# Optimization experiments

Hardware: AMD Instinct MI355X
Metric: run time of the kernel (lower is better)

## Reference

```python
import jax, jax.numpy as jnp
import numpy as np

N_NODES = 50000
N_EDGES = 600000
DIM = 128
VOCAB = 512
PAD_ID = 0
LN_EPS = 1e-5


def setup_inputs() -> dict:
    key = jax.random.key(0)
    ks = jax.random.split(key, 8)
    node_ids = jax.random.randint(ks[0], (N_NODES,), 0, VOCAB, dtype=jnp.int32)
    edge_index = jax.random.randint(ks[1], (2, N_EDGES), 0, N_NODES, dtype=jnp.int32)
    edge_weight = jax.random.uniform(ks[2], (N_EDGES,), dtype=jnp.float32)
    # embedding with padding row zeroed (padding_idx semantics)
    emb = jax.random.normal(ks[3], (VOCAB, DIM), dtype=jnp.float32) * 0.05
    emb = emb.at[PAD_ID].set(0.0)
    s = 1.0 / np.sqrt(DIM)
    W1 = jax.random.normal(ks[4], (DIM, DIM), dtype=jnp.float32) * s
    b1 = jnp.zeros((DIM,), jnp.float32)
    W2 = jax.random.normal(ks[5], (DIM, DIM), dtype=jnp.float32) * s
    b2 = jnp.zeros((DIM,), jnp.float32)
    return {
        "node_ids": node_ids, "edge_index": edge_index, "edge_weight": edge_weight,
        "emb": emb, "W1": W1, "b1": b1, "W2": W2, "b2": b2,
        "gamma1": jnp.ones((DIM,), jnp.float32), "beta1": jnp.zeros((DIM,), jnp.float32),
        "gamma2": jnp.ones((DIM,), jnp.float32), "beta2": jnp.zeros((DIM,), jnp.float32),
    }


def _gcn_conv(x, row, col, ew, W, b, n_nodes):
    """PyG GCNConv: normalize=True, add_self_loops=True, improved=False.
    Aggregation j->i: edge (row=src j, col=dst i)."""
    h = x @ W  # [N, out]
    # add self loops with weight 1
    loop = jnp.arange(n_nodes, dtype=row.dtype)
    row_f = jnp.concatenate([row, loop])
    col_f = jnp.concatenate([col, loop])
    ew_f = jnp.concatenate([ew, jnp.ones((n_nodes,), ew.dtype)])
    # symmetric degree normalization (deg over destination index)
    deg = jax.ops.segment_sum(ew_f, col_f, num_segments=n_nodes)
    dis = jnp.where(deg > 0, jax.lax.rsqrt(jnp.maximum(deg, 1e-12)), 0.0)
    norm = dis[row_f] * ew_f * dis[col_f]  # [E+N]
    msg = norm[:, None] * h[row_f]  # gather + scale  [E+N, out]
    out = jax.ops.segment_sum(msg, col_f, num_segments=n_nodes)  # scatter-add
    return out + b


def _layer_norm(x, gamma, beta):
    mu = jnp.mean(x, axis=-1, keepdims=True)
    var = jnp.mean(jnp.square(x - mu), axis=-1, keepdims=True)
    return (x - mu) * jax.lax.rsqrt(var + LN_EPS) * gamma + beta


def reference(node_ids, edge_index, edge_weight, emb, W1, b1, W2, b2,
              gamma1, beta1, gamma2, beta2):
    row, col = edge_index[0], edge_index[1]
    x = emb[node_ids]  # [N, D]
    x1 = _gcn_conv(x, row, col, edge_weight, W1, b1, N_NODES)
    x = _layer_norm(x + x1, gamma1, beta1)  # dropout is identity in eval
    x2 = _gcn_conv(x, row, col, edge_weight, W2, b2, N_NODES)
    x = _layer_norm(x + x2, gamma2, beta2)
    return x
```

## Files before the change

### kernel.cpp

```cpp
#include <hip/hip_runtime.h>

#define N_NODES 50000
#define N_EDGES 600000
#define DIM     128
#define VOCAB   512
#define LN_EPS  1e-5f
#define FIXS    16777216.0f

typedef unsigned int uint;
typedef unsigned long long ull;

__device__ __forceinline__ uint f2bf(float f) {
    uint u = __float_as_uint(f);
    return (u + 0x7fffu + ((u >> 16) & 1u)) >> 16;
}
__device__ __forceinline__ float bf_lo(uint p) { return __uint_as_float(p << 16); }
__device__ __forceinline__ float bf_hi(uint p) { return __uint_as_float(p & 0xffff0000u); }

__global__ void deg_rank_kernel(const int* __restrict__ ei, const float* __restrict__ ew,
                                ull* pack, int* __restrict__ rank, int E) {
    int e0 = (blockIdx.x * blockDim.x + threadIdx.x) * 4;
    if (e0 >= E) return;
    int4   c = *(const int4*)  (ei + E + e0);
    float4 w = *(const float4*)(ew + e0);
    ull a0 = (1ull << 32) | (ull)(uint)__float2int_rn(w.x * FIXS);
    ull a1 = (1ull << 32) | (ull)(uint)__float2int_rn(w.y * FIXS);
    ull a2 = (1ull << 32) | (ull)(uint)__float2int_rn(w.z * FIXS);
    ull a3 = (1ull << 32) | (ull)(uint)__float2int_rn(w.w * FIXS);
    ull r0 = atomicAdd(&pack[c.x], a0);
    ull r1 = atomicAdd(&pack[c.y], a1);
    ull r2 = atomicAdd(&pack[c.z], a2);
    ull r3 = atomicAdd(&pack[c.w], a3);
    *(int4*)(rank + e0) = make_int4((int)(r0 >> 32), (int)(r1 >> 32),
                                    (int)(r2 >> 32), (int)(r3 >> 32));
}

__global__ void scan_a(const ull* __restrict__ pack,
                       float* dis, int* row_ptr, int* bsum, int n) {
    __shared__ int sd[1024];
    int t = threadIdx.x;
    int i = blockIdx.x * 1024 + t;
    int v = 0;
    if (i < n) {
        ull pv = pack[i];
        v = (int)(pv >> 32);
        dis[i] = rsqrtf(1.0f + (float)(uint)(pv & 0xffffffffu) * (1.0f / FIXS));
    }
    sd[t] = v;
    __syncthreads();
    for (int off = 1; off < 1024; off <<= 1) {
        int add = (t >= off) ? sd[t - off] : 0;
        __syncthreads();
        sd[t] += add;
        __syncthreads();
    }
    if (i < n) row_ptr[i] = sd[t] - v;
    if (t == 1023) bsum[blockIdx.x] = sd[t];
}

__global__ void scan_b(const int* __restrict__ bsum, int* bofs, int nb) {
    int t = threadIdx.x;
    int v = (t < nb) ? bsum[t] : 0;
    int incl = v;
    #pragma unroll
    for (int off = 1; off < 64; off <<= 1) {
        int up = __shfl_up(incl, off, 64);
        if (t >= off) incl += up;
    }
    if (t < nb) bofs[t] = incl - v;
}

__global__ void scan_c(int* row_ptr, const int* __restrict__ bofs, int n, int E) {
    int i = blockIdx.x * 1024 + threadIdx.x;
    if (i < n) row_ptr[i] += bofs[blockIdx.x];
    if (i == 0) row_ptr[n] = E;
}

__global__ void scatter_kernel(const int* __restrict__ ei, const float* __restrict__ ew,
                               const float* __restrict__ dis, const int* __restrict__ nid,
                               const int* __restrict__ row_ptr, const int* __restrict__ rank,
                               int2* __restrict__ epack, int E) {
    int e = blockIdx.x * blockDim.x + threadIdx.x;
    if (e < E) {
        int s = ei[e];
        int c = ei[E + e];
        int pos = row_ptr[c] + rank[e];
        uint ids = (uint)s | ((uint)nid[s] << 16);
        float wp = dis[s] * ew[e];
        epack[pos] = make_int2((int)ids, __float_as_int(wp));
    }
}

template<bool XBF>
__global__ __launch_bounds__(256) void matmul128(const void* __restrict__ Xv,
                                                 const float* __restrict__ W,
                                                 uint* __restrict__ Hb, int M) {
    __shared__ float Wt[32 * 128];
    __shared__ float Xt[64 * 36];
    int tid = threadIdx.x;
    int tx = tid & 31, ty = tid >> 5;
    int r0 = blockIdx.x * 64;
    float acc[8][4];
    #pragma unroll
    for (int j = 0; j < 8; j++)
        #pragma unroll
        for (int c = 0; c < 4; c++) acc[j][c] = 0.f;

    for (int kb = 0; kb < 128; kb += 32) {
        __syncthreads();
        #pragma unroll
        for (int q = 0; q < 4; q++) {
            int f = q * 256 + tid;
            ((float4*)Wt)[f] = *(const float4*)(W + kb * 128 + f * 4);
        }
        #pragma unroll
        for (int q = 0; q < 2; q++) {
            int f = q * 256 + tid;
            int row = f >> 3, cs = f & 7;
            int gr = r0 + row;
            float4 xv = make_float4(0.f, 0.f, 0.f, 0.f);
            if (gr < M) {
                if (XBF) {
                    uint2 xp = *(const uint2*)((const uint*)Xv + (size_t)gr * 64 + kb / 2 + cs * 2);
                    xv = make_float4(bf_lo(xp.x), bf_hi(xp.x), bf_lo(xp.y), bf_hi(xp.y));
                } else {
                    xv = *(const float4*)((const float*)Xv + (size_t)gr * 128 + kb + cs * 4);
                }
            }
            *(float4*)(Xt + row * 36 + cs * 4) = xv;
        }
        __syncthreads();
        #pragma unroll
        for (int k = 0; k < 32; k += 4) {
            float wv[4][4];
            #pragma unroll
            for (int kk = 0; kk < 4; kk++) {
                float4 t4 = *(const float4*)(Wt + (k + kk) * 128 + tx * 4);
                wv[kk][0] = t4.x; wv[kk][1] = t4.y; wv[kk][2] = t4.z; wv[kk][3] = t4.w;
            }
            #pragma unroll
            for (int j = 0; j < 8; j++) {
                float4 xv = *(const float4*)(Xt + (ty * 8 + j) * 36 + k);
                float xs[4] = {xv.x, xv.y, xv.z, xv.w};
                #pragma unroll
                for (int kk = 0; kk < 4; kk++)
                    #pragma unroll
                    for (int c = 0; c < 4; c++)
                        acc[j][c] = fmaf(xs[kk], wv[kk][c], acc[j][c]);
            }
        }
    }
    #pragma unroll
    for (int j = 0; j < 8; j++) {
        int gr = r0 + ty * 8 + j;
        if (gr < M) {
            uint p0 = f2bf(acc[j][0]) | (f2bf(acc[j][1]) << 16);
            uint p1 = f2bf(acc[j][2]) | (f2bf(acc[j][3]) << 16);
            ((uint2*)Hb)[(size_t)gr * 32 + tx] = make_uint2(p0, p1);
        }
    }
}

template<int SHIFT, bool RESID_BF, bool OUT_BF>
__global__ __launch_bounds__(256) void agg_ln(const int* __restrict__ row_ptr,
                                              const int2* __restrict__ epack,
                                              const float* __restrict__ dis,
                                              const uint* __restrict__ hb,
                                              const int* __restrict__ nid,
                                              const void* __restrict__ resid,
                                              const float* __restrict__ bias,
                                              const float* __restrict__ gamma,
                                              const float* __restrict__ beta,
                                              void* __restrict__ out, int n) {
    int i = (blockIdx.x * 256 + threadIdx.x) >> 6;
    int lane = threadIdx.x & 63;
    if (i >= n) return;
    int hri = nid ? nid[i] : i;
    float dl = dis[i];
    uint ps = hb[(size_t)hri * 64 + lane];
    float acc0 = dl * bf_lo(ps);
    float acc1 = dl * bf_hi(ps);
    float c0 = 0.f, c1 = 0.f;
    int e0 = row_ptr[i], e1 = row_ptr[i + 1];
    int j = e0;
    for (; j + 3 < e1; j += 4) {
        int2 r0 = epack[j], r1 = epack[j + 1], r2 = epack[j + 2], r3 = epack[j + 3];
        uint q0 = hb[(size_t)(((uint)r0.x >> SHIFT) & 0xffffu) * 64 + lane];
        uint q1 = hb[(size_t)(((uint)r1.x >> SHIFT) & 0xffffu) * 64 + lane];
        uint q2 = hb[(size_t)(((uint)r2.x >> SHIFT) & 0xffffu) * 64 + lane];
        uint q3 = hb[(size_t)(((uint)r3.x >> SHIFT) & 0xffffu) * 64 + lane];
        float w0 = __int_as_float(r0.y), w1 = __int_as_float(r1.y);
        float w2 = __int_as_float(r2.y), w3 = __int_as_float(r3.y);
        acc0 += w0 * bf_lo(q0); acc1 += w0 * bf_hi(q0);
        c0   += w1 * bf_lo(q1); c1   += w1 * bf_hi(q1);
        acc0 += w2 * bf_lo(q2); acc1 += w2 * bf_hi(q2);
        c0   += w3 * bf_lo(q3); c1   += w3 * bf_hi(q3);
    }
    for (; j < e1; ++j) {
        int2 r = epack[j];
        float w = __int_as_float(r.y);
        uint q = hb[(size_t)(((uint)r.x >> SHIFT) & 0xffffu) * 64 + lane];
        acc0 += w * bf_lo(q); acc1 += w * bf_hi(q);
    }
    acc0 += c0; acc1 += c1;
    float2 xr;
    if (RESID_BF) {
        uint pr = ((const uint*)resid)[(size_t)hri * 64 + lane];
        xr = make_float2(bf_lo(pr), bf_hi(pr));
    } else {
        xr = ((const float2*)resid)[(size_t)hri * 64 + lane];
    }
    float2 bi = ((const float2*)bias)[lane];
    float v0 = xr.x + dl * acc0 + bi.x;
    float v1 = xr.y + dl * acc1 + bi.y;
    float s1 = v0 + v1, s2 = v0 * v0 + v1 * v1;
    #pragma unroll
    for (int o = 32; o > 0; o >>= 1) {
        s1 += __shfl_xor(s1, o, 64);
        s2 += __shfl_xor(s2, o, 64);
    }
    float mu   = s1 * (1.0f / DIM);
    float var  = s2 * (1.0f / DIM) - mu * mu;
    float rstd = rsqrtf(var + LN_EPS);
    float2 ga = ((const float2*)gamma)[lane];
    float2 be = ((const float2*)beta)[lane];
    float o0 = (v0 - mu) * rstd * ga.x + be.x;
    float o1 = (v1 - mu) * rstd * ga.y + be.y;
    if (OUT_BF) {
        ((uint*)out)[(size_t)i * 64 + lane] = f2bf(o0) | (f2bf(o1) << 16);
    } else {
        ((float2*)out)[(size_t)i * 64 + lane] = make_float2(o0, o1);
    }
}

extern "C" void kernel_launch(void* const* d_in, const int* in_sizes, int n_in,
                              void* d_out, int out_size, void* d_ws, size_t ws_size,
                              hipStream_t stream) {
    const int*   node_ids = (const int*)  d_in[0];
    const int*   ei       = (const int*)  d_in[1];
    const float* ew       = (const float*)d_in[2];
    const float* emb      = (const float*)d_in[3];
    const float* W1       = (const float*)d_in[4];
    const float* b1       = (const float*)d_in[5];
    const float* W2       = (const float*)d_in[6];
    const float* b2       = (const float*)d_in[7];
    const float* g1       = (const float*)d_in[8];
    const float* be1      = (const float*)d_in[9];
    const float* g2       = (const float*)d_in[10];
    const float* be2      = (const float*)d_in[11];
    float* out = (float*)d_out;

    char* p = (char*)d_ws;
    auto alloc = [&](size_t bytes) {
        char* r = p;
        p += (bytes + 255) & ~(size_t)255;
        return r;
    };
    uint*  h2b     = (uint*) alloc((size_t)N_NODES * 64 * 4);
    uint*  x1b     = (uint*) alloc((size_t)N_NODES * 64 * 4);
    uint*  hembB   = (uint*) alloc((size_t)VOCAB * 64 * 4);
    ull*   pack    = (ull*)  alloc((size_t)N_NODES * 8);
    float* disv    = (float*)alloc((size_t)N_NODES * 4);
    int*   row_ptr = (int*)  alloc((size_t)(N_NODES + 1) * 4);
    int*   rank    = (int*)  alloc((size_t)N_EDGES * 4);
    int*   bsum    = (int*)  alloc(64 * 4);
    int*   bofs    = (int*)  alloc(64 * 4);
    int2*  epack   = (int2*) alloc((size_t)N_EDGES * 8);

    int nb = (N_NODES + 1023) / 1024;

    hipMemsetAsync(pack, 0, (size_t)N_NODES * 8, stream);
    deg_rank_kernel<<<(N_EDGES / 4 + 255) / 256, 256, 0, stream>>>(ei, ew, pack, rank, N_EDGES);
    scan_a<<<nb, 1024, 0, stream>>>(pack, disv, row_ptr, bsum, N_NODES);
    scan_b<<<1, 64, 0, stream>>>(bsum, bofs, nb);
    scan_c<<<nb, 1024, 0, stream>>>(row_ptr, bofs, N_NODES, N_EDGES);
    scatter_kernel<<<(N_EDGES + 255) / 256, 256, 0, stream>>>(ei, ew, disv, node_ids,
                                                              row_ptr, rank, epack, N_EDGES);

    matmul128<false><<<(VOCAB + 63) / 64, 256, 0, stream>>>(emb, W1, hembB, VOCAB);
    agg_ln<16, false, true><<<(N_NODES + 3) / 4, 256, 0, stream>>>(
        row_ptr, epack, disv, hembB, node_ids, emb, b1, g1, be1, x1b, N_NODES);

    matmul128<true><<<(N_NODES + 63) / 64, 256, 0, stream>>>(x1b, W2, h2b, N_NODES);
    agg_ln<0, true, false><<<(N_NODES + 3) / 4, 256, 0, stream>>>(
        row_ptr, epack, disv, h2b, nullptr, x1b, b2, g2, be2, out, N_NODES);
}
```

Baseline: 252.2 us.

## Use bf16 MFMA for second-layer matmul and widen aggregation gather batching

Replaces the FP32 shared-memory SIMT matmul for the 50000x128x128 second-layer projection with a bf16 MFMA kernel. W2 is prepacked into an MFMA-friendly bf16 layout by a small extra kernel, and the already-bf16 activations are fed directly. The aggregation loop now issues 8 edge-record and gather loads per iteration, with masked tails and 4 independent accumulators, to expose more memory-level parallelism. W2 is quantised to bf16, which adds rounding error. The MFMA kernel also writes output as scattered 2-byte stores.

Measured after the change: 242.2 us. -3.9%, faster.

```diff
diff --git a/kernel.cpp b/kernel.cpp
--- a/kernel.cpp
+++ b/kernel.cpp
@@ -9,6 +9,9 @@
 
 typedef unsigned int uint;
 typedef unsigned long long ull;
+typedef unsigned short ushort;
+typedef __attribute__((ext_vector_type(8))) short s8v;
+typedef __attribute__((ext_vector_type(4))) float f4v;
 
 __device__ __forceinline__ uint f2bf(float f) {
     uint u = __float_as_uint(f);
@@ -91,8 +94,16 @@
     }
 }
 
-template<bool XBF>
-__global__ __launch_bounds__(256) void matmul128(const void* __restrict__ Xv,
+__global__ void prepack_w(const float* __restrict__ W, ushort* __restrict__ Wp) {
+    int o = blockIdx.x * 256 + threadIdx.x;
+    int j = o & 7, lane = (o >> 3) & 63, chunk = o >> 9;
+    int kc = chunk & 3, nc = chunk >> 2;
+    int k = kc * 32 + (lane >> 4) * 8 + j;
+    int n = nc * 16 + (lane & 15);
+    Wp[o] = (ushort)f2bf(W[k * 128 + n]);
+}
+
+__global__ __launch_bounds__(256) void matmul128(const float* __restrict__ X,
                                                  const float* __restrict__ W,
                                                  uint* __restrict__ Hb, int M) {
     __shared__ float Wt[32 * 128];
@@ -119,14 +130,7 @@
             int row = f >> 3, cs = f & 7;
             int gr = r0 + row;
             float4 xv = make_float4(0.f, 0.f, 0.f, 0.f);
-            if (gr < M) {
-                if (XBF) {
-                    uint2 xp = *(const uint2*)((const uint*)Xv + (size_t)gr * 64 + kb / 2 + cs * 2);
-                    xv = make_float4(bf_lo(xp.x), bf_hi(xp.x), bf_lo(xp.y), bf_hi(xp.y));
-                } else {
-                    xv = *(const float4*)((const float*)Xv + (size_t)gr * 128 + kb + cs * 4);
-                }
-            }
+            if (gr < M) xv = *(const float4*)(X + (size_t)gr * 128 + kb + cs * 4);
             *(float4*)(Xt + row * 36 + cs * 4) = xv;
         }
         __syncthreads();
@@ -161,6 +165,33 @@
     }
 }
 
+__global__ __launch_bounds__(256) void mm2_mfma(const uint* __restrict__ Xb,
+                                                const ushort* __restrict__ Wp,
+                                                ushort* __restrict__ H, int M) {
+    int wid = (blockIdx.x * 256 + threadIdx.x) >> 6;
+    int lane = threadIdx.x & 63;
+    int r0 = wid * 16;
+    if (r0 >= M) return;
+    int quad = lane >> 4, lo = lane & 15;
+    const uint* xrow = Xb + (size_t)(r0 + lo) * 64 + quad * 4;
+    s8v a[4];
+    #pragma unroll
+    for (int kc = 0; kc < 4; kc++) a[kc] = *(const s8v*)(xrow + kc * 16);
+    #pragma unroll
+    for (int nc = 0; nc < 8; nc++) {
+        f4v acc = {0.f, 0.f, 0.f, 0.f};
+        #pragma unroll
+        for (int kc = 0; kc < 4; kc++) {
+            s8v b = *(const s8v*)(Wp + (size_t)((nc * 4 + kc) * 64 + lane) * 8);
+            acc = __builtin_amdgcn_mfma_f32_16x16x32_bf16(a[kc], b, acc, 0, 0, 0);
+        }
+        ushort* hp = H + (size_t)(r0 + quad * 4) * 128 + nc * 16 + lo;
+        #pragma unroll
+        for (int r = 0; r < 4; r++)
+            hp[(size_t)r * 128] = (ushort)f2bf(acc[r]);
+    }
+}
+
 template<int SHIFT, bool RESID_BF, bool OUT_BF>
 __global__ __launch_bounds__(256) void agg_ln(const int* __restrict__ row_ptr,
                                               const int2* __restrict__ epack,
@@ -178,31 +209,29 @@
     int hri = nid ? nid[i] : i;
     float dl = dis[i];
     uint ps = hb[(size_t)hri * 64 + lane];
-    float acc0 = dl * bf_lo(ps);
-    float acc1 = dl * bf_hi(ps);
-    float c0 = 0.f, c1 = 0.f;
+    float sx[4] = {dl * bf_lo(ps), 0.f, 0.f, 0.f};
+    float sy[4] = {dl * bf_hi(ps), 0.f, 0.f, 0.f};
     int e0 = row_ptr[i], e1 = row_ptr[i + 1];
-    int j = e0;
-    for (; j + 3 < e1; j += 4) {
-        int2 r0 = epack[j], r1 = epack[j + 1], r2 = epack[j + 2], r3 = epack[j + 3];
-        uint q0 = hb[(size_t)(((uint)r0.x >> SHIFT) & 0xffffu) * 64 + lane];
-        uint q1 = hb[(size_t)(((uint)r1.x >> SHIFT) & 0xffffu) * 64 + lane];
-        uint q2 = hb[(size_t)(((uint)r2.x >> SHIFT) & 0xffffu) * 64 + lane];
-        uint q3 = hb[(size_t)(((uint)r3.x >> SHIFT) & 0xffffu) * 64 + lane];
-        float w0 = __int_as_float(r0.y), w1 = __int_as_float(r1.y);
-        float w2 = __int_as_float(r2.y), w3 = __int_as_float(r3.y);
-        acc0 += w0 * bf_lo(q0); acc1 += w0 * bf_hi(q0);
-        c0   += w1 * bf_lo(q1); c1   += w1 * bf_hi(q1);
-        acc0 += w2 * bf_lo(q2); acc1 += w2 * bf_hi(q2);
-        c0   += w3 * bf_lo(q3); c1   += w3 * bf_hi(q3);
-    }
-    for (; j < e1; ++j) {
-        int2 r = epack[j];
-        float w = __int_as_float(r.y);
-        uint q = hb[(size_t)(((uint)r.x >> SHIFT) & 0xffffu) * 64 + lane];
-        acc0 += w * bf_lo(q); acc1 += w * bf_hi(q);
-    }
-    acc0 += c0; acc1 += c1;
+    for (int j = e0; j < e1; j += 8) {
+        int2 er[8];
+        #pragma unroll
+        for (int k = 0; k < 8; k++) {
+            int idx = (j + k < e1) ? j + k : e0;
+            er[k] = epack[idx];
+        }
+        uint qv[8];
+        #pragma unroll
+        for (int k = 0; k < 8; k++)
+            qv[k] = hb[(size_t)(((uint)er[k].x >> SHIFT) & 0xffffu) * 64 + lane];
+        #pragma unroll
+        for (int k = 0; k < 8; k++) {
+            float w = (j + k < e1) ? __int_as_float(er[k].y) : 0.f;
+            sx[k & 3] += w * bf_lo(qv[k]);
+            sy[k & 3] += w * bf_hi(qv[k]);
+        }
+    }
+    float acc0 = (sx[0] + sx[1]) + (sx[2] + sx[3]);
+    float acc1 = (sy[0] + sy[1]) + (sy[2] + sy[3]);
     float2 xr;
     if (RESID_BF) {
         uint pr = ((const uint*)resid)[(size_t)hri * 64 + lane];
@@ -256,16 +285,17 @@
         p += (bytes + 255) & ~(size_t)255;
         return r;
     };
-    uint*  h2b     = (uint*) alloc((size_t)N_NODES * 64 * 4);
-    uint*  x1b     = (uint*) alloc((size_t)N_NODES * 64 * 4);
-    uint*  hembB   = (uint*) alloc((size_t)VOCAB * 64 * 4);
-    ull*   pack    = (ull*)  alloc((size_t)N_NODES * 8);
-    float* disv    = (float*)alloc((size_t)N_NODES * 4);
-    int*   row_ptr = (int*)  alloc((size_t)(N_NODES + 1) * 4);
-    int*   rank    = (int*)  alloc((size_t)N_EDGES * 4);
-    int*   bsum    = (int*)  alloc(64 * 4);
-    int*   bofs    = (int*)  alloc(64 * 4);
-    int2*  epack   = (int2*) alloc((size_t)N_EDGES * 8);
+    uint*   h2b     = (uint*)  alloc((size_t)N_NODES * 64 * 4);
+    uint*   x1b     = (uint*)  alloc((size_t)N_NODES * 64 * 4);
+    uint*   hembB   = (uint*)  alloc((size_t)VOCAB * 64 * 4);
+    ushort* Wp      = (ushort*)alloc((size_t)128 * 128 * 2);
+    ull*    pack    = (ull*)   alloc((size_t)N_NODES * 8);
+    float*  disv    = (float*) alloc((size_t)N_NODES * 4);
+    int*    row_ptr = (int*)   alloc((size_t)(N_NODES + 1) * 4);
+    int*    rank    = (int*)   alloc((size_t)N_EDGES * 4);
+    int*    bsum    = (int*)   alloc(64 * 4);
+    int*    bofs    = (int*)   alloc(64 * 4);
+    int2*   epack   = (int2*)  alloc((size_t)N_EDGES * 8);
 
     int nb = (N_NODES + 1023) / 1024;
 
@@ -276,12 +306,13 @@
     scan_c<<<nb, 1024, 0, stream>>>(row_ptr, bofs, N_NODES, N_EDGES);
     scatter_kernel<<<(N_EDGES + 255) / 256, 256, 0, stream>>>(ei, ew, disv, node_ids,
                                                               row_ptr, rank, epack, N_EDGES);
-
-    matmul128<false><<<(VOCAB + 63) / 64, 256, 0, stream>>>(emb, W1, hembB, VOCAB);
+    prepack_w<<<64, 256, 0, stream>>>(W2, Wp);
+
+    matmul128<<<(VOCAB + 63) / 64, 256, 0, stream>>>(emb, W1, hembB, VOCAB);
     agg_ln<16, false, true><<<(N_NODES + 3) / 4, 256, 0, stream>>>(
         row_ptr, epack, disv, hembB, node_ids, emb, b1, g1, be1, x1b, N_NODES);
 
-    matmul128<true><<<(N_NODES + 63) / 64, 256, 0, stream>>>(x1b, W2, h2b, N_NODES);
+    mm2_mfma<<<(N_NODES / 16 + 3) / 4, 256, 0, stream>>>(x1b, Wp, (ushort*)h2b, N_NODES);
     agg_ln<0, true, false><<<(N_NODES + 3) / 4, 256, 0, stream>>>(
         row_ptr, epack, disv, h2b, nullptr, x1b, b2, g2, be2, out, N_NODES);
 }
```
